# Kernel optimization log

Hardware: AMD Instinct MI355X
Metric: run time of the kernel (lower is better)

## Reference

```python
import jax, jax.numpy as jnp
import numpy as np

B = 32768
DNA, IMG, FUSED, HEADS = 768, 512, 256, 4
HEAD_DIM = FUSED // HEADS
GENUS, SPECIES, MAXSP = 372, 1050, 23
RED, GEMB, SDH, DEC_HID = 128, 64, 64, 744


def setup_inputs() -> dict:
    key = jax.random.key(0)
    ks = iter(jax.random.split(key, 40))
    p = lambda *shape: jax.random.normal(next(ks), shape, jnp.float32) * 0.02
    z = lambda n: jnp.zeros((n,), jnp.float32)
    inp = {
        'dna_emb': jax.random.normal(next(ks), (B, DNA), jnp.float32),
        'img_emb': jax.random.normal(next(ks), (B, IMG), jnp.float32),
        # AttentionFusion params
        'W_dna': p(DNA, FUSED), 'b_dna': z(FUSED),
        'W_img': p(IMG, FUSED), 'b_img': z(FUSED),
        'W_qkv': p(FUSED, 3 * FUSED), 'b_qkv': z(3 * FUSED),
        'W_o': p(FUSED, FUSED), 'b_o': z(FUSED),
        'W_f1': p(FUSED, FUSED), 'b_f1': z(FUSED),
        'W_f2': p(FUSED, FUSED), 'b_f2': z(FUSED),
        # genus Decoder params
        'W_d1': p(FUSED, DEC_HID), 'b_d1': z(DEC_HID),
        'W_d2': p(DEC_HID, GENUS), 'b_d2': z(GENUS),
        # SpeciePredictor params
        'W_fp': p(FUSED, RED), 'b_fp': z(RED),
        'W_ge': p(GENUS, GEMB), 'b_ge': z(GEMB),
        'W_s1': p(RED + GEMB, SDH), 'b_s1': z(SDH),
        'W_s2': p(SDH, MAXSP), 'b_s2': z(MAXSP),
        # precomputed scatter->gather indices: species s -> (genus s%372, local s//372)
        'species_genus': jnp.arange(SPECIES, dtype=jnp.int32) % GENUS,
        'species_local': jnp.arange(SPECIES, dtype=jnp.int32) // GENUS,
    }
    return inp


def _forward(dna_emb, img_emb, W_dna, b_dna, W_img, b_img, W_qkv, b_qkv, W_o, b_o,
             W_f1, b_f1, W_f2, b_f2, W_d1, b_d1, W_d2, b_d2, W_fp, b_fp,
             W_ge, b_ge, W_s1, b_s1, W_s2, b_s2, species_genus, species_local):
    # --- AttentionFusion ---
    dna_proj = dna_emb @ W_dna + b_dna                     # [B, F]
    img_proj = img_emb @ W_img + b_img                     # [B, F]
    seq = jnp.stack([dna_proj, img_proj], axis=1)          # [B, 2, F]
    qkv = seq @ W_qkv + b_qkv                              # [B, 2, 3F]
    q, k, v = jnp.split(qkv, 3, axis=-1)
    q = q.reshape(B, 2, HEADS, HEAD_DIM)
    k = k.reshape(B, 2, HEADS, HEAD_DIM)
    v = v.reshape(B, 2, HEADS, HEAD_DIM)
    scale = 1.0 / np.sqrt(HEAD_DIM).astype(np.float32)
    scores = jnp.einsum('bqhd,bkhd->bhqk', q, k) * scale   # [B, H, 2, 2]
    attn = jax.nn.softmax(scores, axis=-1)
    ctx = jnp.einsum('bhqk,bkhd->bqhd', attn, v).reshape(B, 2, FUSED)
    attn_out = ctx @ W_o + b_o                             # [B, 2, F]
    fused = attn_out.mean(axis=1)                          # [B, F]
    fused = jax.nn.relu(fused @ W_f1 + b_f1) @ W_f2 + b_f2
    # --- genus Decoder (Linear -> Sigmoid -> Linear -> softmax) ---
    genus_logits = jax.nn.softmax(
        jax.nn.sigmoid(fused @ W_d1 + b_d1) @ W_d2 + b_d2, axis=1)  # [B, 372]
    # --- species head ---
    reduced_fused = fused @ W_fp + b_fp                    # [B, 128]
    genus_emb = genus_logits @ W_ge + b_ge                 # [B, 64]
    genus_fused = jnp.concatenate([genus_emb, reduced_fused], axis=1)  # [B, 192]
    local_logits = jax.nn.sigmoid(genus_fused @ W_s1 + b_s1) @ W_s2 + b_s2  # [B, 23]
    # --- _flatten_species_probs_batch, fused: result[:, s] = genus_logits[:, g(s)] * local_logits[:, l(s)]
    # (avoids materializing the [B, 372, 23] outer product)
    species_probs = genus_logits[:, species_genus] * local_logits[:, species_local]  # [B, 1050]
    return species_probs, local_logits, genus_logits, fused, reduced_fused


def reference(dna_emb, img_emb, W_dna, b_dna, W_img, b_img, W_qkv, b_qkv, W_o, b_o,
              W_f1, b_f1, W_f2, b_f2, W_d1, b_d1, W_d2, b_d2, W_fp, b_fp,
              W_ge, b_ge, W_s1, b_s1, W_s2, b_s2, species_genus, species_local):
    return _forward(dna_emb, img_emb, W_dna, b_dna, W_img, b_img, W_qkv, b_qkv,
                    W_o, b_o, W_f1, b_f1, W_f2, b_f2, W_d1, b_d1, W_d2, b_d2,
                    W_fp, b_fp, W_ge, b_ge, W_s1, b_s1, W_s2, b_s2,
                    species_genus, species_local)
```

## Files before the change

### kernel.cpp

```cpp
#include <hip/hip_runtime.h>
#include <hip/hip_bf16.h>

typedef __hip_bfloat16 bf16;
typedef __attribute__((ext_vector_type(8))) short short8_t;
typedef __attribute__((ext_vector_type(4))) float f32x4;

#define B_ROWS 32768

__device__ __forceinline__ float to_f(float x) { return x; }
__device__ __forceinline__ float to_f(bf16 x) { return __bfloat162float(x); }

__device__ __forceinline__ unsigned short f2bf(float f) {
    union { float f; unsigned int u; } c; c.f = f;
    unsigned int u = c.u;
    unsigned int rb = ((u >> 16) & 1u) + 0x7fffu;
    return (unsigned short)((u + rb) >> 16);
}

__device__ __forceinline__ void glds16(const void* g, void* s) {
    __builtin_amdgcn_global_load_lds(
        (const __attribute__((address_space(1))) unsigned int*)g,
        (__attribute__((address_space(3))) unsigned int*)s, 16, 0, 0);
}

__device__ __forceinline__ void stage8f(const float* __restrict__ src, bf16* dst) {
    const float4 a = *(const float4*)src;
    const float4 b = *(const float4*)(src + 4);
    union { uint4 u; unsigned short h[8]; } r;
    r.h[0] = f2bf(a.x); r.h[1] = f2bf(a.y); r.h[2] = f2bf(a.z); r.h[3] = f2bf(a.w);
    r.h[4] = f2bf(b.x); r.h[5] = f2bf(b.y); r.h[6] = f2bf(b.z); r.h[7] = f2bf(b.w);
    *(uint4*)dst = r.u;
}

template <typename TA, int BN, int ACT>
__global__ __launch_bounds__(BN * 2) void gemm_mfma(
    const TA* __restrict__ A, int lda,
    const bf16* __restrict__ Wt, int kpad,
    const float* __restrict__ bias,
    float* __restrict__ outf, int ldof,
    bf16* __restrict__ outb, int ldob,
    int M, int N, int nstore, int K)
{
    constexpr int NT = BN * 2;
    constexpr int WC = BN / 64;
    __shared__ __align__(16) bf16 As[128 * 64];
    __shared__ __align__(16) bf16 Bs[BN * 64];

    const int tid = threadIdx.x;
    const int lane = tid & 63;
    const int w = tid >> 6;
    const int wr = w / WC, wc = w % WC;
    const int m0 = blockIdx.y * 128, n0 = blockIdx.x * BN;
    const int kq = lane >> 4, lr = lane & 15;

    f32x4 acc[4][4] = {};

    for (int k0 = 0; k0 < K; k0 += 64) {
        if constexpr (sizeof(TA) == 2) {
#pragma unroll
            for (int j = 0; j < 1024 / NT; ++j) {
                const int c = tid + j * NT;
                const int row = c >> 3, sx = (c & 7) ^ (row & 7);
                glds16(A + (size_t)(m0 + row) * lda + k0 + sx * 8, &As[c * 8]);
            }
        } else {
#pragma unroll
            for (int j = 0; j < 1024 / NT; ++j) {
                const int c = tid + j * NT;
                const int row = c >> 3, sx = (c & 7) ^ (row & 7);
                stage8f(A + (size_t)(m0 + row) * lda + k0 + (c & 7) * 8,
                        &As[row * 64 + sx * 8]);
            }
        }
#pragma unroll
        for (int j = 0; j < BN * 8 / NT; ++j) {
            const int c = tid + j * NT;
            const int row = c >> 3, sx = (c & 7) ^ (row & 7);
            glds16(Wt + (size_t)(n0 + row) * kpad + k0 + sx * 8, &Bs[c * 8]);
        }
        __syncthreads();
#pragma unroll
        for (int kk = 0; kk < 2; ++kk) {
            const int co = ((kk * 4 + kq) ^ (lr & 7)) << 3;
            short8_t am[4], wf[4];
#pragma unroll
            for (int i = 0; i < 4; ++i) {
                am[i] = *(const short8_t*)&As[(wr * 64 + i * 16 + lr) * 64 + co];
                wf[i] = *(const short8_t*)&Bs[(wc * 64 + i * 16 + lr) * 64 + co];
            }
#pragma unroll
            for (int i = 0; i < 4; ++i)
#pragma unroll
                for (int j = 0; j < 4; ++j)
                    acc[i][j] = __builtin_amdgcn_mfma_f32_16x16x32_bf16(
                        wf[j], am[i], acc[i][j], 0, 0, 0);
        }
        __syncthreads();
    }

#pragma unroll
    for (int mi = 0; mi < 4; ++mi) {
        const size_t m = m0 + wr * 64 + mi * 16 + lr;
#pragma unroll
        for (int ni = 0; ni < 4; ++ni) {
            const int nb = n0 + wc * 64 + ni * 16 + 4 * kq;
            if (nb >= nstore) continue;
            float vv[4];
#pragma unroll
            for (int r = 0; r < 4; ++r) {
                const int n = nb + r;
                float v = acc[mi][ni][r] + ((n < N) ? bias[n] : 0.f);
                if (ACT == 1) v = fmaxf(v, 0.f);
                if (ACT == 2) v = (n < N) ? 1.f / (1.f + __expf(-v)) : 0.f;
                vv[r] = v;
            }
            if (outf) {
                if (nb + 3 < N) {
                    float4 f4; f4.x = vv[0]; f4.y = vv[1]; f4.z = vv[2]; f4.w = vv[3];
                    *(float4*)&outf[m * ldof + nb] = f4;
                } else {
#pragma unroll
                    for (int r = 0; r < 4; ++r)
                        if (nb + r < N) outf[m * ldof + nb + r] = vv[r];
                }
            }
            if (outb) {
                if (nb + 3 < nstore) {
                    union { uint2 u; unsigned short h[4]; } pk;
                    pk.h[0] = f2bf(vv[0]); pk.h[1] = f2bf(vv[1]);
                    pk.h[2] = f2bf(vv[2]); pk.h[3] = f2bf(vv[3]);
                    *(uint2*)&outb[m * ldob + nb] = pk.u;
                } else {
#pragma unroll
                    for (int r = 0; r < 4; ++r)
                        if (nb + r < nstore)
                            ((unsigned short*)outb)[m * ldob + nb + r] = f2bf(vv[r]);
                }
            }
        }
    }
}

#define MLP3_STAGE_W(WP)                                                       \
    _Pragma("unroll")                                                          \
    for (int j = 0; j < 4; ++j) {                                              \
        const int c = tid + j * 512;                                           \
        const int row = c >> 3, sx = (c & 7) ^ (row & 7);                      \
        glds16(WP + (size_t)row * 256 + ks * 64 + sx * 8, &Wb[c * 8]);         \
    }

#define MLP3_COMPUTE(ASRC)                                                     \
    _Pragma("unroll")                                                          \
    for (int kk = 0; kk < 2; ++kk) {                                           \
        const int co = ((kk * 4 + kq) ^ (lr & 7)) << 3;                        \
        short8_t am[4], wf[4];                                                 \
        _Pragma("unroll")                                                      \
        for (int i = 0; i < 4; ++i) {                                          \
            am[i] = *(const short8_t*)&(ASRC)[(wr * 64 + i * 16 + lr) * 64 + co]; \
            wf[i] = *(const short8_t*)&Wb[(wc * 64 + i * 16 + lr) * 64 + co];  \
        }                                                                      \
        _Pragma("unroll")                                                      \
        for (int i = 0; i < 4; ++i)                                            \
            _Pragma("unroll")                                                  \
            for (int j2 = 0; j2 < 4; ++j2)                                     \
                acc[i][j2] = __builtin_amdgcn_mfma_f32_16x16x32_bf16(          \
                    wf[j2], am[i], acc[i][j2], 0, 0, 0);                       \
    }

#define MLP3_STORE_T(BIASP, RELU)                                              \
    _Pragma("unroll")                                                          \
    for (int mi = 0; mi < 4; ++mi) {                                           \
        const int m = wr * 64 + mi * 16 + lr;                                  \
        _Pragma("unroll")                                                      \
        for (int ni = 0; ni < 4; ++ni) {                                       \
            const int nb = wc * 64 + ni * 16 + 4 * kq;                         \
            union { unsigned long long u; unsigned short h[4]; } pk;           \
            _Pragma("unroll")                                                  \
            for (int r = 0; r < 4; ++r) {                                      \
                float v = acc[mi][ni][r] + BIASP[nb + r];                      \
                if (RELU) v = fmaxf(v, 0.f);                                   \
                pk.h[r] = f2bf(v);                                             \
            }                                                                  \
            *(unsigned long long*)&T[nb >> 6]                                  \
                [m * 64 + ((((nb & 63) >> 3) ^ (m & 7)) << 3) + (nb & 7)] = pk.u; \
        }                                                                      \
    }

#define ZERO_ACC                                                               \
    _Pragma("unroll")                                                          \
    for (int i = 0; i < 4; ++i)                                                \
        _Pragma("unroll")                                                      \
        for (int j2 = 0; j2 < 4; ++j2) acc[i][j2] = f32x4{0.f, 0.f, 0.f, 0.f};

__global__ __launch_bounds__(512) void mlp3_kernel(
    const bf16* __restrict__ ctxm,
    const bf16* __restrict__ Wo, const float* __restrict__ b_o,
    const bf16* __restrict__ Wf1, const float* __restrict__ b_f1,
    const bf16* __restrict__ Wf2, const float* __restrict__ b_f2,
    float* __restrict__ o_fused, bf16* __restrict__ fbuf)
{
    __shared__ __align__(16) bf16 Ab[128 * 64];
    __shared__ __align__(16) bf16 Wb[256 * 64];
    __shared__ __align__(16) bf16 T[4][128 * 64];

    const int tid = threadIdx.x, lane = tid & 63, w = tid >> 6;
    const int wr = w >> 2, wc = w & 3;
    const int m0 = blockIdx.x * 128;
    const int kq = lane >> 4, lr = lane & 15;

    f32x4 acc[4][4];
    ZERO_ACC

    for (int ks = 0; ks < 4; ++ks) {
#pragma unroll
        for (int j = 0; j < 2; ++j) {
            const int c = tid + j * 512;
            const int row = c >> 3, sx = (c & 7) ^ (row & 7);
            glds16(ctxm + (size_t)(m0 + row) * 256 + ks * 64 + sx * 8, &Ab[c * 8]);
        }
        MLP3_STAGE_W(Wo)
        __syncthreads();
        MLP3_COMPUTE(Ab)
        __syncthreads();
    }
    MLP3_STORE_T(b_o, false)
    __syncthreads();

    ZERO_ACC
    for (int ks = 0; ks < 4; ++ks) {
        MLP3_STAGE_W(Wf1)
        __syncthreads();
        MLP3_COMPUTE(T[ks])
        __syncthreads();
    }
    MLP3_STORE_T(b_f1, true)
    __syncthreads();

    ZERO_ACC
    for (int ks = 0; ks < 4; ++ks) {
        MLP3_STAGE_W(Wf2)
        __syncthreads();
        MLP3_COMPUTE(T[ks])
        __syncthreads();
    }
#pragma unroll
    for (int mi = 0; mi < 4; ++mi) {
        const size_t m = m0 + wr * 64 + mi * 16 + lr;
#pragma unroll
        for (int ni = 0; ni < 4; ++ni) {
            const int nb = wc * 64 + ni * 16 + 4 * kq;
            float vv[4];
            union { unsigned long long u; unsigned short h[4]; } pk;
#pragma unroll
            for (int r = 0; r < 4; ++r) {
                vv[r] = acc[mi][ni][r] + b_f2[nb + r];
                pk.h[r] = f2bf(vv[r]);
            }
            float4 f4; f4.x = vv[0]; f4.y = vv[1]; f4.z = vv[2]; f4.w = vv[3];
            *(float4*)&o_fused[m * 256 + nb] = f4;
            *(unsigned long long*)&fbuf[m * 256 + nb] = pk.u;
        }
    }
}

struct PrepackArgs {
    const float* src[12];
    unsigned long long off[12];
    int K[12], N[12], Kpad[12], Nr[12];
};

__global__ __launch_bounds__(256) void prepack_kernel(PrepackArgs a, bf16* wsbase)
{
    const int wI = blockIdx.y;
    const float* __restrict__ src = a.src[wI];
    bf16* dst = wsbase + a.off[wI];
    const int K = a.K[wI], N = a.N[wI], Kpad = a.Kpad[wI];
    const int tilesK = Kpad >> 6, tilesN = a.Nr[wI] >> 6;
    __shared__ float tile[64][65];

    for (int t = blockIdx.x; t < tilesK * tilesN; t += gridDim.x) {
        const int k0 = (t % tilesK) << 6, n0 = (t / tilesK) << 6;
        const int cc = threadIdx.x & 63, rr = threadIdx.x >> 6;
#pragma unroll
        for (int i = 0; i < 16; ++i) {
            const int k = k0 + rr + i * 4, n = n0 + cc;
            tile[rr + i * 4][cc] = (k < K && n < N) ? src[(size_t)k * N + n] : 0.f;
        }
        __syncthreads();
#pragma unroll
        for (int i = 0; i < 16; ++i) {
            const int nl = rr + i * 4;
            ((unsigned short*)dst)[(size_t)(n0 + nl) * Kpad + k0 + cc] =
                f2bf(tile[cc][nl]);
        }
        __syncthreads();
    }
}

__global__ __launch_bounds__(256) void attn_kernel(
    const bf16* __restrict__ qkv, bf16* __restrict__ ctxm)
{
    const int b = blockIdx.x;
    const int lane = threadIdx.x & 63;
    const bf16* base = qkv + (size_t)b * 1536;
    const int o = (threadIdx.x >> 6) * 64 + lane;

    float q0 = to_f(base[o]),       k0 = to_f(base[256 + o]),       v0 = to_f(base[512 + o]);
    float q1 = to_f(base[768 + o]), k1 = to_f(base[768 + 256 + o]), v1 = to_f(base[768 + 512 + o]);

    float s00 = q0 * k0, s01 = q0 * k1, s10 = q1 * k0, s11 = q1 * k1;
#pragma unroll
    for (int off = 32; off; off >>= 1) {
        s00 += __shfl_xor(s00, off);
        s01 += __shfl_xor(s01, off);
        s10 += __shfl_xor(s10, off);
        s11 += __shfl_xor(s11, off);
    }
    const float sc = 0.125f;
    s00 *= sc; s01 *= sc; s10 *= sc; s11 *= sc;

    float m0 = fmaxf(s00, s01);
    float e00 = __expf(s00 - m0), e01 = __expf(s01 - m0);
    float r0 = 1.f / (e00 + e01);
    float m1 = fmaxf(s10, s11);
    float e10 = __expf(s10 - m1), e11 = __expf(s11 - m1);
    float r1 = 1.f / (e10 + e11);

    float c0 = e00 * r0 * v0 + e01 * r0 * v1;
    float c1 = e10 * r1 * v0 + e11 * r1 * v1;
    ctxm[(size_t)b * 256 + o] = __float2bfloat16(0.5f * (c0 + c1));
}

__global__ __launch_bounds__(64) void softmax372_kernel(
    const bf16* __restrict__ in, float* __restrict__ outf, bf16* __restrict__ outb)
{
    const int b = blockIdx.x;
    const int lane = threadIdx.x;
    const bf16* row = in + (size_t)b * 372;

    float v[6];
    float mx = -1e30f;
#pragma unroll
    for (int i = 0; i < 6; ++i) {
        int idx = lane + i * 64;
        v[i] = (idx < 372) ? to_f(row[idx]) : -1e30f;
        mx = fmaxf(mx, v[i]);
    }
#pragma unroll
    for (int off = 32; off; off >>= 1) mx = fmaxf(mx, __shfl_xor(mx, off));

    float s = 0.f;
#pragma unroll
    for (int i = 0; i < 6; ++i) {
        int idx = lane + i * 64;
        if (idx < 372) { v[i] = __expf(v[i] - mx); s += v[i]; }
    }
#pragma unroll
    for (int off = 32; off; off >>= 1) s += __shfl_xor(s, off);
    float r = 1.f / s;

#pragma unroll
    for (int i = 0; i < 6; ++i) {
        int idx = lane + i * 64;
        if (idx < 372) {
            float p = v[i] * r;
            outf[(size_t)b * 372 + idx] = p;
            outb[(size_t)b * 384 + idx] = __float2bfloat16(p);
        } else if (idx < 384) {
            outb[(size_t)b * 384 + idx] = __float2bfloat16(0.f);
        }
    }
}

__global__ __launch_bounds__(256) void species_kernel(
    const float* __restrict__ g, const float* __restrict__ ll,
    const int* __restrict__ sg, const int* __restrict__ sl,
    float* __restrict__ out)
{
    const int s = blockIdx.x * 256 + threadIdx.x;
    const int b = blockIdx.y;
    if (s < 1050) {
        out[(size_t)b * 1050 + s] =
            g[(size_t)b * 372 + sg[s]] * ll[(size_t)b * 23 + sl[s]];
    }
}

extern "C" void kernel_launch(void* const* d_in, const int* in_sizes, int n_in,
                              void* d_out, int out_size, void* d_ws, size_t ws_size,
                              hipStream_t stream)
{
    const int B = B_ROWS;
    const float* dna   = (const float*)d_in[0];
    const float* img   = (const float*)d_in[1];
    const float* W_dna = (const float*)d_in[2];  const float* b_dna = (const float*)d_in[3];
    const float* W_img = (const float*)d_in[4];  const float* b_img = (const float*)d_in[5];
    const float* W_qkv = (const float*)d_in[6];  const float* b_qkv = (const float*)d_in[7];
    const float* W_o   = (const float*)d_in[8];  const float* b_o   = (const float*)d_in[9];
    const float* W_f1  = (const float*)d_in[10]; const float* b_f1  = (const float*)d_in[11];
    const float* W_f2  = (const float*)d_in[12]; const float* b_f2  = (const float*)d_in[13];
    const float* W_d1  = (const float*)d_in[14]; const float* b_d1  = (const float*)d_in[15];
    const float* W_d2  = (const float*)d_in[16]; const float* b_d2  = (const float*)d_in[17];
    const float* W_fp  = (const float*)d_in[18]; const float* b_fp  = (const float*)d_in[19];
    const float* W_ge  = (const float*)d_in[20]; const float* b_ge  = (const float*)d_in[21];
    const float* W_s1  = (const float*)d_in[22]; const float* b_s1  = (const float*)d_in[23];
    const float* W_s2  = (const float*)d_in[24]; const float* b_s2  = (const float*)d_in[25];
    const int*   sg    = (const int*)d_in[26];
    const int*   sl    = (const int*)d_in[27];

    bf16* ws = (bf16*)d_ws;

    static const int KK[12] = {768, 512, 256, 256, 256, 256, 256, 744, 256, 372, 192, 64};
    static const int NN[12] = {256, 256, 768, 256, 256, 256, 744, 372, 128,  64,  64, 23};
    const float* SRC[12] = {W_dna, W_img, W_qkv, W_o, W_f1, W_f2, W_d1, W_d2, W_fp, W_ge, W_s1, W_s2};
    PrepackArgs pa;
    size_t woff[12];
    size_t off = 0;
    for (int i = 0; i < 12; ++i) {
        pa.src[i] = SRC[i]; pa.K[i] = KK[i]; pa.N[i] = NN[i];
        pa.Kpad[i] = (KK[i] + 63) & ~63;
        pa.Nr[i]   = (NN[i] + 255) & ~255;
        pa.off[i] = off; woff[i] = off;
        off += (size_t)pa.Kpad[i] * pa.Nr[i];
    }
    const size_t AOFF = off;

    bf16* seq  = ws + AOFF;
    bf16* qkvf = ws + AOFF + (size_t)B * 512;
    bf16* ctxm = ws + AOFF;
    bf16* fbuf = ws + AOFF + (size_t)B * 256;
    bf16* h1   = ws + AOFF + (size_t)B * 512;
    bf16* g    = ws + AOFF + (size_t)B * 1280;
    bf16* gbf  = ws + AOFF + (size_t)B * 512;
    bf16* gf   = ws + AOFF + (size_t)B * 896;
    bf16* sh   = ws + AOFF + (size_t)B * 1088;

    float* out       = (float*)d_out;
    float* o_species = out;
    float* o_local   = out + (size_t)B * 1050;
    float* o_genus   = out + (size_t)B * 1073;
    float* o_fused   = out + (size_t)B * 1445;
    float* o_red     = out + (size_t)B * 1701;

    prepack_kernel<<<dim3(64, 12), 256, 0, stream>>>(pa, ws);

#define NOF (float*)nullptr, 0
#define NOB (bf16*)nullptr, 0

    gemm_mfma<float, 256, 0><<<dim3(1, 256), 512, 0, stream>>>(
        dna, 768, ws + woff[0], 768, b_dna, NOF, seq, 512, B, 256, 256, 768);
    gemm_mfma<float, 256, 0><<<dim3(1, 256), 512, 0, stream>>>(
        img, 512, ws + woff[1], 512, b_img, NOF, seq + 256, 512, B, 256, 256, 512);
    gemm_mfma<bf16, 256, 0><<<dim3(3, 512), 512, 0, stream>>>(
        seq, 256, ws + woff[2], 256, b_qkv, NOF, qkvf, 768, 2 * B, 768, 768, 256);
    attn_kernel<<<B, 256, 0, stream>>>(qkvf, ctxm);
    mlp3_kernel<<<256, 512, 0, stream>>>(
        ctxm, ws + woff[3], b_o, ws + woff[4], b_f1, ws + woff[5], b_f2,
        o_fused, fbuf);
    gemm_mfma<bf16, 256, 2><<<dim3(3, 256), 512, 0, stream>>>(
        fbuf, 256, ws + woff[6], 256, b_d1, NOF, h1, 768, B, 744, 768, 256);
    gemm_mfma<bf16, 256, 0><<<dim3(2, 256), 512, 0, stream>>>(
        h1, 768, ws + woff[7], 768, b_d2, NOF, g, 372, B, 372, 372, 768);
    softmax372_kernel<<<B, 64, 0, stream>>>(g, o_genus, gbf);
    gemm_mfma<bf16, 128, 0><<<dim3(1, 256), 256, 0, stream>>>(
        gbf, 384, ws + woff[9], 384, b_ge, NOF, gf, 192, B, 64, 64, 384);
    gemm_mfma<bf16, 128, 0><<<dim3(1, 256), 256, 0, stream>>>(
        fbuf, 256, ws + woff[8], 256, b_fp, o_red, 128, gf + 64, 192, B, 128, 128, 256);
    gemm_mfma<bf16, 128, 2><<<dim3(1, 256), 256, 0, stream>>>(
        gf, 192, ws + woff[10], 192, b_s1, NOF, sh, 64, B, 64, 64, 192);
    gemm_mfma<bf16, 128, 0><<<dim3(1, 256), 256, 0, stream>>>(
        sh, 64, ws + woff[11], 64, b_s2, o_local, 23, NOB, B, 23, 23, 64);
    species_kernel<<<dim3(5, B), 256, 0, stream>>>(o_genus, o_local, sg, sl, o_species);
#undef NOF
#undef NOB
}
```

Measured before the change: 804.1 us.

## Double-buffer GEMM LDS, pre-convert fp32 inputs, batch rows in small kernels

The GEMM now uses two LDS buffers, so the next K tile is loaded with async global-to-LDS copies while the current one is computed, and it drops one barrier per step. The fp32 inputs are converted to bf16 by a separate kernel, so every GEMM can take the async load path. Attention and softmax kernels now handle four rows per block, and the species kernel becomes a flat grid-stride loop. The cost is an extra fp32 read and bf16 write of the inputs, double the LDS per block (which may lower occupancy), and a larger workspace.

```diff
diff --git a/kernel.cpp b/kernel.cpp
--- a/kernel.cpp
+++ b/kernel.cpp
@@ -23,7 +23,7 @@
         (__attribute__((address_space(3))) unsigned int*)s, 16, 0, 0);
 }
 
-__device__ __forceinline__ void stage8f(const float* __restrict__ src, bf16* dst) {
+__device__ __forceinline__ void cvt8(const float* __restrict__ src, bf16* dst) {
     const float4 a = *(const float4*)src;
     const float4 b = *(const float4*)(src + 4);
     union { uint4 u; unsigned short h[8]; } r;
@@ -32,9 +32,20 @@
     *(uint4*)dst = r.u;
 }
 
-template <typename TA, int BN, int ACT>
+__global__ __launch_bounds__(256) void cvt_kernel(
+    const float* __restrict__ a, bf16* __restrict__ oa, int ca,
+    const float* __restrict__ b, bf16* __restrict__ ob, int cb)
+{
+    const int total = ca + cb;
+    for (int e = blockIdx.x * 256 + threadIdx.x; e < total; e += gridDim.x * 256) {
+        if (e < ca) cvt8(a + (size_t)e * 8, oa + (size_t)e * 8);
+        else        cvt8(b + (size_t)(e - ca) * 8, ob + (size_t)(e - ca) * 8);
+    }
+}
+
+template <int BN, int ACT>
 __global__ __launch_bounds__(BN * 2) void gemm_mfma(
-    const TA* __restrict__ A, int lda,
+    const bf16* __restrict__ A, int lda,
     const bf16* __restrict__ Wt, int kpad,
     const float* __restrict__ bias,
     float* __restrict__ outf, int ldof,
@@ -43,8 +54,8 @@
 {
     constexpr int NT = BN * 2;
     constexpr int WC = BN / 64;
-    __shared__ __align__(16) bf16 As[128 * 64];
-    __shared__ __align__(16) bf16 Bs[BN * 64];
+    __shared__ __align__(16) bf16 As[2][128 * 64];
+    __shared__ __align__(16) bf16 Bs[2][BN * 64];
 
     const int tid = threadIdx.x;
     const int lane = tid & 63;
@@ -55,38 +66,30 @@
 
     f32x4 acc[4][4] = {};
 
-    for (int k0 = 0; k0 < K; k0 += 64) {
-        if constexpr (sizeof(TA) == 2) {
-#pragma unroll
-            for (int j = 0; j < 1024 / NT; ++j) {
-                const int c = tid + j * NT;
-                const int row = c >> 3, sx = (c & 7) ^ (row & 7);
-                glds16(A + (size_t)(m0 + row) * lda + k0 + sx * 8, &As[c * 8]);
-            }
-        } else {
-#pragma unroll
-            for (int j = 0; j < 1024 / NT; ++j) {
-                const int c = tid + j * NT;
-                const int row = c >> 3, sx = (c & 7) ^ (row & 7);
-                stage8f(A + (size_t)(m0 + row) * lda + k0 + (c & 7) * 8,
-                        &As[row * 64 + sx * 8]);
-            }
+    auto stage = [&](int t, int pb) {
+        const int kb = t * 64;
+#pragma unroll
+        for (int j = 0; j < 1024 / NT; ++j) {
+            const int c = tid + j * NT;
+            const int row = c >> 3, sx = (c & 7) ^ (row & 7);
+            glds16(A + (size_t)(m0 + row) * lda + kb + sx * 8, &As[pb][c * 8]);
         }
 #pragma unroll
         for (int j = 0; j < BN * 8 / NT; ++j) {
             const int c = tid + j * NT;
             const int row = c >> 3, sx = (c & 7) ^ (row & 7);
-            glds16(Wt + (size_t)(n0 + row) * kpad + k0 + sx * 8, &Bs[c * 8]);
-        }
-        __syncthreads();
+            glds16(Wt + (size_t)(n0 + row) * kpad + kb + sx * 8, &Bs[pb][c * 8]);
+        }
+    };
+    auto compute = [&](int pb) {
 #pragma unroll
         for (int kk = 0; kk < 2; ++kk) {
             const int co = ((kk * 4 + kq) ^ (lr & 7)) << 3;
             short8_t am[4], wf[4];
 #pragma unroll
             for (int i = 0; i < 4; ++i) {
-                am[i] = *(const short8_t*)&As[(wr * 64 + i * 16 + lr) * 64 + co];
-                wf[i] = *(const short8_t*)&Bs[(wc * 64 + i * 16 + lr) * 64 + co];
+                am[i] = *(const short8_t*)&As[pb][(wr * 64 + i * 16 + lr) * 64 + co];
+                wf[i] = *(const short8_t*)&Bs[pb][(wc * 64 + i * 16 + lr) * 64 + co];
             }
 #pragma unroll
             for (int i = 0; i < 4; ++i)
@@ -95,6 +98,14 @@
                     acc[i][j] = __builtin_amdgcn_mfma_f32_16x16x32_bf16(
                         wf[j], am[i], acc[i][j], 0, 0, 0);
         }
+    };
+
+    const int nsteps = K >> 6;
+    stage(0, 0);
+    __syncthreads();
+    for (int t = 0; t < nsteps; ++t) {
+        if (t + 1 < nsteps) stage(t + 1, (t + 1) & 1);
+        compute(t & 1);
         __syncthreads();
     }
 
@@ -300,42 +311,45 @@
 __global__ __launch_bounds__(256) void attn_kernel(
     const bf16* __restrict__ qkv, bf16* __restrict__ ctxm)
 {
-    const int b = blockIdx.x;
     const int lane = threadIdx.x & 63;
-    const bf16* base = qkv + (size_t)b * 1536;
     const int o = (threadIdx.x >> 6) * 64 + lane;
-
-    float q0 = to_f(base[o]),       k0 = to_f(base[256 + o]),       v0 = to_f(base[512 + o]);
-    float q1 = to_f(base[768 + o]), k1 = to_f(base[768 + 256 + o]), v1 = to_f(base[768 + 512 + o]);
-
-    float s00 = q0 * k0, s01 = q0 * k1, s10 = q1 * k0, s11 = q1 * k1;
-#pragma unroll
-    for (int off = 32; off; off >>= 1) {
-        s00 += __shfl_xor(s00, off);
-        s01 += __shfl_xor(s01, off);
-        s10 += __shfl_xor(s10, off);
-        s11 += __shfl_xor(s11, off);
-    }
-    const float sc = 0.125f;
-    s00 *= sc; s01 *= sc; s10 *= sc; s11 *= sc;
-
-    float m0 = fmaxf(s00, s01);
-    float e00 = __expf(s00 - m0), e01 = __expf(s01 - m0);
-    float r0 = 1.f / (e00 + e01);
-    float m1 = fmaxf(s10, s11);
-    float e10 = __expf(s10 - m1), e11 = __expf(s11 - m1);
-    float r1 = 1.f / (e10 + e11);
-
-    float c0 = e00 * r0 * v0 + e01 * r0 * v1;
-    float c1 = e10 * r1 * v0 + e11 * r1 * v1;
-    ctxm[(size_t)b * 256 + o] = __float2bfloat16(0.5f * (c0 + c1));
-}
-
-__global__ __launch_bounds__(64) void softmax372_kernel(
+#pragma unroll
+    for (int sI = 0; sI < 4; ++sI) {
+        const int b = blockIdx.x * 4 + sI;
+        const bf16* base = qkv + (size_t)b * 1536;
+
+        float q0 = to_f(base[o]),       k0 = to_f(base[256 + o]),       v0 = to_f(base[512 + o]);
+        float q1 = to_f(base[768 + o]), k1 = to_f(base[768 + 256 + o]), v1 = to_f(base[768 + 512 + o]);
+
+        float s00 = q0 * k0, s01 = q0 * k1, s10 = q1 * k0, s11 = q1 * k1;
+#pragma unroll
+        for (int off = 32; off; off >>= 1) {
+            s00 += __shfl_xor(s00, off);
+            s01 += __shfl_xor(s01, off);
+            s10 += __shfl_xor(s10, off);
+            s11 += __shfl_xor(s11, off);
+        }
+        const float sc = 0.125f;
+        s00 *= sc; s01 *= sc; s10 *= sc; s11 *= sc;
+
+        float m0 = fmaxf(s00, s01);
+        float e00 = __expf(s00 - m0), e01 = __expf(s01 - m0);
+        float r0 = 1.f / (e00 + e01);
+        float m1 = fmaxf(s10, s11);
+        float e10 = __expf(s10 - m1), e11 = __expf(s11 - m1);
+        float r1 = 1.f / (e10 + e11);
+
+        float c0 = e00 * r0 * v0 + e01 * r0 * v1;
+        float c1 = e10 * r1 * v0 + e11 * r1 * v1;
+        ctxm[(size_t)b * 256 + o] = __float2bfloat16(0.5f * (c0 + c1));
+    }
+}
+
+__global__ __launch_bounds__(256) void softmax372_kernel(
     const bf16* __restrict__ in, float* __restrict__ outf, bf16* __restrict__ outb)
 {
-    const int b = blockIdx.x;
-    const int lane = threadIdx.x;
+    const int b = blockIdx.x * 4 + (threadIdx.x >> 6);
+    const int lane = threadIdx.x & 63;
     const bf16* row = in + (size_t)b * 372;
 
     float v[6];
@@ -377,11 +391,10 @@
     const int* __restrict__ sg, const int* __restrict__ sl,
     float* __restrict__ out)
 {
-    const int s = blockIdx.x * 256 + threadIdx.x;
-    const int b = blockIdx.y;
-    if (s < 1050) {
-        out[(size_t)b * 1050 + s] =
-            g[(size_t)b * 372 + sg[s]] * ll[(size_t)b * 23 + sl[s]];
+    const int total = B_ROWS * 1050;
+    for (int e = blockIdx.x * 256 + threadIdx.x; e < total; e += gridDim.x * 256) {
+        const int b = e / 1050, s = e - b * 1050;
+        out[e] = g[(size_t)b * 372 + sg[s]] * ll[(size_t)b * 23 + sl[s]];
     }
 }
 
@@ -424,15 +437,17 @@
     }
     const size_t AOFF = off;
 
-    bf16* seq  = ws + AOFF;
-    bf16* qkvf = ws + AOFF + (size_t)B * 512;
+    bf16* dnab = ws + AOFF;
+    bf16* imgb = ws + AOFF + (size_t)B * 768;
+    bf16* seq  = ws + AOFF + (size_t)B * 1280;
+    bf16* qkvf = ws + AOFF + (size_t)B * 1792;
     bf16* ctxm = ws + AOFF;
     bf16* fbuf = ws + AOFF + (size_t)B * 256;
     bf16* h1   = ws + AOFF + (size_t)B * 512;
     bf16* g    = ws + AOFF + (size_t)B * 1280;
-    bf16* gbf  = ws + AOFF + (size_t)B * 512;
-    bf16* gf   = ws + AOFF + (size_t)B * 896;
-    bf16* sh   = ws + AOFF + (size_t)B * 1088;
+    bf16* gbf  = ws + AOFF + (size_t)B * 1792;
+    bf16* gf   = ws + AOFF + (size_t)B * 2176;
+    bf16* sh   = ws + AOFF + (size_t)B * 2368;
 
     float* out       = (float*)d_out;
     float* o_species = out;
@@ -442,34 +457,35 @@
     float* o_red     = out + (size_t)B * 1701;
 
     prepack_kernel<<<dim3(64, 12), 256, 0, stream>>>(pa, ws);
+    cvt_kernel<<<2048, 256, 0, stream>>>(dna, dnab, B * 96, img, imgb, B * 64);
 
 #define NOF (float*)nullptr, 0
 #define NOB (bf16*)nullptr, 0
 
-    gemm_mfma<float, 256, 0><<<dim3(1, 256), 512, 0, stream>>>(
-        dna, 768, ws + woff[0], 768, b_dna, NOF, seq, 512, B, 256, 256, 768);
-    gemm_mfma<float, 256, 0><<<dim3(1, 256), 512, 0, stream>>>(
-        img, 512, ws + woff[1], 512, b_img, NOF, seq + 256, 512, B, 256, 256, 512);
-    gemm_mfma<bf16, 256, 0><<<dim3(3, 512), 512, 0, stream>>>(
+    gemm_mfma<256, 0><<<dim3(1, 256), 512, 0, stream>>>(
+        dnab, 768, ws + woff[0], 768, b_dna, NOF, seq, 512, B, 256, 256, 768);
+    gemm_mfma<256, 0><<<dim3(1, 256), 512, 0, stream>>>(
+        imgb, 512, ws + woff[1], 512, b_img, NOF, seq + 256, 512, B, 256, 256, 512);
+    gemm_mfma<256, 0><<<dim3(3, 512), 512, 0, stream>>>(
         seq, 256, ws + woff[2], 256, b_qkv, NOF, qkvf, 768, 2 * B, 768, 768, 256);
-    attn_kernel<<<B, 256, 0, stream>>>(qkvf, ctxm);
+    attn_kernel<<<B / 4, 256, 0, stream>>>(qkvf, ctxm);
     mlp3_kernel<<<256, 512, 0, stream>>>(
         ctxm, ws + woff[3], b_o, ws + woff[4], b_f1, ws + woff[5], b_f2,
         o_fused, fbuf);
-    gemm_mfma<bf16, 256, 2><<<dim3(3, 256), 512, 0, stream>>>(
+    gemm_mfma<256, 2><<<dim3(3, 256), 512, 0, stream>>>(
         fbuf, 256, ws + woff[6], 256, b_d1, NOF, h1, 768, B, 744, 768, 256);
-    gemm_mfma<bf16, 256, 0><<<dim3(2, 256), 512, 0, stream>>>(
+    gemm_mfma<256, 0><<<dim3(2, 256), 512, 0, stream>>>(
         h1, 768, ws + woff[7], 768, b_d2, NOF, g, 372, B, 372, 372, 768);
-    softmax372_kernel<<<B, 64, 0, stream>>>(g, o_genus, gbf);
-    gemm_mfma<bf16, 128, 0><<<dim3(1, 256), 256, 0, stream>>>(
+    softmax372_kernel<<<B / 4, 256, 0, stream>>>(g, o_genus, gbf);
+    gemm_mfma<128, 0><<<dim3(1, 256), 256, 0, stream>>>(
         gbf, 384, ws + woff[9], 384, b_ge, NOF, gf, 192, B, 64, 64, 384);
-    gemm_mfma<bf16, 128, 0><<<dim3(1, 256), 256, 0, stream>>>(
+    gemm_mfma<128, 0><<<dim3(1, 256), 256, 0, stream>>>(
         fbuf, 256, ws + woff[8], 256, b_fp, o_red, 128, gf + 64, 192, B, 128, 128, 256);
-    gemm_mfma<bf16, 128, 2><<<dim3(1, 256), 256, 0, stream>>>(
+    gemm_mfma<128, 2><<<dim3(1, 256), 256, 0, stream>>>(
         gf, 192, ws + woff[10], 192, b_s1, NOF, sh, 64, B, 64, 64, 192);
-    gemm_mfma<bf16, 128, 0><<<dim3(1, 256), 256, 0, stream>>>(
+    gemm_mfma<128, 0><<<dim3(1, 256), 256, 0, stream>>>(
         sh, 64, ws + woff[11], 64, b_s2, o_local, 23, NOB, B, 23, 23, 64);
-    species_kernel<<<dim3(5, B), 256, 0, stream>>>(o_genus, o_local, sg, sl, o_species);
+    species_kernel<<<4096, 256, 0, stream>>>(o_genus, o_local, sg, sl, o_species);
 #undef NOF
 #undef NOB
 }
```

Result: slower. 873.2 us (+8.6%).
